# Optimization experiments

Hardware: AMD Instinct MI355X
Metric: run time of the kernel (lower is better)

## Reference

```python
import jax, jax.numpy as jnp
import numpy as np

N = 100000   # nodes
DIM = 128    # feature dim
E = 800000   # edges per hop
K = 4        # hops
BN_EPS = 1e-5


def setup_inputs() -> dict:
    key = jax.random.key(0)
    ks = jax.random.split(key, 24)
    inp = {}
    for i in range(K):
        inp[f"x{i}"] = jax.random.normal(ks[i], (N, DIM), dtype=jnp.float32)
    inp["edge_attr"] = jax.random.normal(ks[4], (E, DIM), dtype=jnp.float32)
    for i in range(K):
        inp[f"e{i}"] = jax.random.randint(ks[5 + i], (2, E), 0, N, dtype=jnp.int32)
    s1 = 1.0 / np.sqrt(DIM)
    s2 = 1.0 / np.sqrt(2 * DIM)
    inp["W1"] = jax.random.uniform(ks[9], (DIM, 2 * DIM), jnp.float32, -s1, s1)
    inp["b1"] = jax.random.uniform(ks[10], (2 * DIM,), jnp.float32, -s1, s1)
    inp["bn1_g"] = jnp.ones((2 * DIM,), jnp.float32)
    inp["bn1_b"] = jnp.zeros((2 * DIM,), jnp.float32)
    inp["W2"] = jax.random.uniform(ks[11], (2 * DIM, DIM), jnp.float32, -s2, s2)
    inp["b2"] = jax.random.uniform(ks[12], (DIM,), jnp.float32, -s2, s2)
    inp["bn2_g"] = jnp.ones((DIM,), jnp.float32)
    inp["bn2_b"] = jnp.zeros((DIM,), jnp.float32)
    inp["bn3_g"] = jnp.ones((DIM,), jnp.float32)
    inp["bn3_b"] = jnp.zeros((DIM,), jnp.float32)
    inp["eps_param"] = jnp.zeros((K + 1, DIM), jnp.float32)  # nn.Parameter(zeros)
    return inp


def _bn(h, g, b):
    # BatchNorm1d, train-mode math: batch mean / biased var per feature
    m = jnp.mean(h, axis=0)
    v = jnp.var(h, axis=0)
    return g * (h - m) * jax.lax.rsqrt(v + BN_EPS) + b


def _propagate(x, edge_index, edge_attr):
    # message: relu(x_j [+ edge_attr]); aggregate: scatter-add at dst
    msg = x[edge_index[0]]                      # [E, DIM] gather from src
    if edge_attr is not None:
        msg = msg + edge_attr
    msg = jax.nn.relu(msg)
    return jax.ops.segment_sum(msg, edge_index[1], num_segments=N)


def reference(x0, x1, x2, x3, edge_attr, e0, e1, e2, e3,
              W1, b1, bn1_g, bn1_b, W2, b2, bn2_g, bn2_b,
              bn3_g, bn3_b, eps_param):
    xs = [x0, x1, x2, x3]
    es = [e0, e1, e2, e3]
    result = (1.0 + eps_param[0]) * x0
    for i in range(K):
        ea = edge_attr if i == 0 else None
        result = result + (1.0 + eps_param[i + 1]) * _propagate(xs[i], es[i], ea)
    # GIN MLP: Linear -> BN -> ReLU -> Linear -> BN -> ReLU
    h = jax.nn.relu(_bn(result @ W1 + b1, bn1_g, bn1_b))
    h = jax.nn.relu(_bn(h @ W2 + b2, bn2_g, bn2_b))
    # outer ConvBlock: BN -> act (relu, not last layer); dropout in eval = identity
    h = jax.nn.relu(_bn(h, bn3_g, bn3_b))
    return h  # new x[0]; original also carries XX through unchanged
```

## Files before the change

### kernel.cpp

```cpp
#include <hip/hip_runtime.h>
#include <cstdint>
#include <cstddef>

#define NN 100000
#define D 128
#define NE 800000
#define BN_EPS 1e-5f

#define M4 (4 * NN)
#define CH 1000
#define NB 400
#define G64 1563

typedef __attribute__((ext_vector_type(4))) float f32x4;
typedef __attribute__((ext_vector_type(8))) short s16x8;

__device__ inline unsigned short f2bf(float f) {
  unsigned int u = __builtin_bit_cast(unsigned int, f);
  u += 0x7FFFu + ((u >> 16) & 1u);
  return (unsigned short)(u >> 16);
}

__global__ __launch_bounds__(256) void k_prep(const float* __restrict__ W1,
                                              const float* __restrict__ W2,
                                              unsigned short* __restrict__ W1T,
                                              unsigned short* __restrict__ W2T) {
  int i = blockIdx.x * 256 + threadIdx.x;
  if (i >= 32768) return;
  int k1 = i >> 8, n1 = i & 255;
  W1T[n1 * 128 + k1] = f2bf(W1[i]);
  int k2 = i >> 7, n2 = i & 127;
  W2T[n2 * 256 + k2] = f2bf(W2[i]);
}

__global__ __launch_bounds__(256) void k_count(
    const int* __restrict__ e0, const int* __restrict__ e1,
    const int* __restrict__ e2, const int* __restrict__ e3,
    unsigned int* __restrict__ pcount, unsigned char* __restrict__ wrank) {
  const int h = blockIdx.y;
  const int* e = h == 0 ? e0 : h == 1 ? e1 : h == 2 ? e2 : e3;
  const int eid = blockIdx.x * 256 + threadIdx.x;
  const int dst = e[NE + eid];
  unsigned int old = atomicAdd(&pcount[dst], 1u << (8 * h));
  wrank[h * NE + eid] = (unsigned char)((old >> (8 * h)) & 0xFFu);
}

__global__ __launch_bounds__(256) void k_scanA(const unsigned int* __restrict__ pcount,
                                               int* __restrict__ bsum) {
  __shared__ int red[256];
  const int b = blockIdx.x, t = threadIdx.x;
  int s = 0;
  if (t < 250) {
    unsigned int p = pcount[b * 250 + t];
    s = (int)((p & 0xFFu) + ((p >> 8) & 0xFFu) + ((p >> 16) & 0xFFu) + (p >> 24));
  }
  red[t] = s; __syncthreads();
  for (int off = 128; off > 0; off >>= 1) {
    if (t < off) red[t] += red[t + off];
    __syncthreads();
  }
  if (t == 0) bsum[b] = red[0];
}

__global__ __launch_bounds__(512) void k_scanB(const int* __restrict__ bsum,
                                               int* __restrict__ bpre) {
  __shared__ int s[512];
  const int t = threadIdx.x;
  const int v = (t < NB) ? bsum[t] : 0;
  s[t] = v; __syncthreads();
  for (int off = 1; off < 512; off <<= 1) {
    int x = s[t];
    if (t >= off) x += s[t - off];
    __syncthreads(); s[t] = x; __syncthreads();
  }
  if (t < NB) bpre[t] = s[t] - v;
}

__global__ __launch_bounds__(256) void k_scanC(const unsigned int* __restrict__ pcount,
                                               const int* __restrict__ bpre,
                                               int* __restrict__ offsets) {
  __shared__ int cnt[CH];
  __shared__ int part[256];
  const int b = blockIdx.x, t = threadIdx.x;
  if (t < 250) {
    unsigned int p = pcount[b * 250 + t];
    cnt[t * 4 + 0] = (int)(p & 0xFFu);
    cnt[t * 4 + 1] = (int)((p >> 8) & 0xFFu);
    cnt[t * 4 + 2] = (int)((p >> 16) & 0xFFu);
    cnt[t * 4 + 3] = (int)(p >> 24);
  }
  __syncthreads();
  int own = 0;
#pragma unroll
  for (int j = 0; j < 4; j++) {
    int idx = t * 4 + j;
    if (idx < CH) own += cnt[idx];
  }
  part[t] = own; __syncthreads();
  for (int off = 1; off < 256; off <<= 1) {
    int x = part[t];
    if (t >= off) x += part[t - off];
    __syncthreads(); part[t] = x; __syncthreads();
  }
  int run = bpre[b] + part[t] - own;
#pragma unroll
  for (int j = 0; j < 4; j++) {
    int idx = t * 4 + j;
    if (idx < CH) { offsets[b * CH + idx] = run; run += cnt[idx]; }
  }
  if (b == 0 && t == 0) offsets[M4] = 4 * NE;
}

__global__ __launch_bounds__(256) void k_place(
    const int* __restrict__ e0, const int* __restrict__ e1,
    const int* __restrict__ e2, const int* __restrict__ e3,
    const int* __restrict__ offsets, const unsigned char* __restrict__ wrank,
    int* __restrict__ srcs, int* __restrict__ eids) {
  const int h = blockIdx.y;
  const int* e = h == 0 ? e0 : h == 1 ? e1 : h == 2 ? e2 : e3;
  const int eid = blockIdx.x * 256 + threadIdx.x;
  const int src = e[eid];
  const int dst = e[NE + eid];
  const int pos = offsets[dst * 4 + h] + (int)wrank[h * NE + eid];
  srcs[pos] = src;
  if (h == 0) eids[pos] = eid;
}

__global__ __launch_bounds__(256) void k_gather(
    const float* __restrict__ x0, const float* __restrict__ x1,
    const float* __restrict__ x2, const float* __restrict__ x3,
    const float* __restrict__ edge_attr, const float* __restrict__ eps,
    const int* __restrict__ offsets, const int* __restrict__ srcs,
    const int* __restrict__ eids, unsigned short* __restrict__ result) {
  const int dst  = blockIdx.x * 4 + (threadIdx.x >> 6);
  const int lane = threadIdx.x & 63;
  const int d    = lane * 2;

  const int4 ob = *reinterpret_cast<const int4*>(offsets + 4 * dst);
  const int o0 = ob.x, b1 = ob.y, b2 = ob.z, b3 = ob.w;
  const int o4 = offsets[4 * dst + 4];

  float2 h0 = make_float2(0.f, 0.f);
  float2 h1 = make_float2(0.f, 0.f);
  float2 h2 = make_float2(0.f, 0.f);
  float2 h3 = make_float2(0.f, 0.f);

  {
    int j = o0;
    for (; j + 2 <= b1; j += 2) {
      const int p0 = srcs[j],     p1 = srcs[j + 1];
      const int q0 = eids[j],     q1 = eids[j + 1];
      float2 v0 = *reinterpret_cast<const float2*>(x0 + p0 * D + d);
      float2 w0 = *reinterpret_cast<const float2*>(edge_attr + (size_t)q0 * D + d);
      float2 v1 = *reinterpret_cast<const float2*>(x0 + p1 * D + d);
      float2 w1 = *reinterpret_cast<const float2*>(edge_attr + (size_t)q1 * D + d);
      h0.x += fmaxf(v0.x + w0.x, 0.f); h0.y += fmaxf(v0.y + w0.y, 0.f);
      h0.x += fmaxf(v1.x + w1.x, 0.f); h0.y += fmaxf(v1.y + w1.y, 0.f);
    }
    if (j < b1) {
      const int p = srcs[j];
      const int q = eids[j];
      float2 v = *reinterpret_cast<const float2*>(x0 + p * D + d);
      float2 w = *reinterpret_cast<const float2*>(edge_attr + (size_t)q * D + d);
      h0.x += fmaxf(v.x + w.x, 0.f); h0.y += fmaxf(v.y + w.y, 0.f);
    }
  }

#define HOP_LOOP(XP, ACC, BEG, END) do {                                       \
    int j_ = (BEG);                                                            \
    for (; j_ + 4 <= (END); j_ += 4) {                                         \
      const int p0_ = srcs[j_], p1_ = srcs[j_ + 1];                            \
      const int p2_ = srcs[j_ + 2], p3_ = srcs[j_ + 3];                        \
      float2 v0_ = *reinterpret_cast<const float2*>((XP) + p0_ * D + d);       \
      float2 v1_ = *reinterpret_cast<const float2*>((XP) + p1_ * D + d);       \
      float2 v2_ = *reinterpret_cast<const float2*>((XP) + p2_ * D + d);       \
      float2 v3_ = *reinterpret_cast<const float2*>((XP) + p3_ * D + d);       \
      ACC.x += fmaxf(v0_.x, 0.f); ACC.y += fmaxf(v0_.y, 0.f);                  \
      ACC.x += fmaxf(v1_.x, 0.f); ACC.y += fmaxf(v1_.y, 0.f);                  \
      ACC.x += fmaxf(v2_.x, 0.f); ACC.y += fmaxf(v2_.y, 0.f);                  \
      ACC.x += fmaxf(v3_.x, 0.f); ACC.y += fmaxf(v3_.y, 0.f);                  \
    }                                                                          \
    for (; j_ < (END); ++j_) {                                                 \
      const int p_ = srcs[j_];                                                 \
      float2 v_ = *reinterpret_cast<const float2*>((XP) + p_ * D + d);         \
      ACC.x += fmaxf(v_.x, 0.f); ACC.y += fmaxf(v_.y, 0.f);                    \
    }                                                                          \
  } while (0)

  HOP_LOOP(x1, h1, b1, b2);
  HOP_LOOP(x2, h2, b2, b3);
  HOP_LOOP(x3, h3, b3, o4);
#undef HOP_LOOP

  float2 e0v = *reinterpret_cast<const float2*>(eps + d);
  float2 s1 = *reinterpret_cast<const float2*>(eps + 1 * D + d);
  float2 s2 = *reinterpret_cast<const float2*>(eps + 2 * D + d);
  float2 s3 = *reinterpret_cast<const float2*>(eps + 3 * D + d);
  float2 s4 = *reinterpret_cast<const float2*>(eps + 4 * D + d);
  float2 xv = *reinterpret_cast<const float2*>(x0 + dst * D + d);

  float ax = (1.f + e0v.x) * xv.x + (1.f + s1.x) * h0.x + (1.f + s2.x) * h1.x
           + (1.f + s3.x) * h2.x + (1.f + s4.x) * h3.x;
  float ay = (1.f + e0v.y) * xv.y + (1.f + s1.y) * h0.y + (1.f + s2.y) * h1.y
           + (1.f + s3.y) * h2.y + (1.f + s4.y) * h3.y;

  reinterpret_cast<unsigned int*>(result)[dst * 64 + lane] =
      (unsigned int)f2bf(ax) | ((unsigned int)f2bf(ay) << 16);
}

__global__ __launch_bounds__(256) void k_gemm1(const unsigned short* __restrict__ Ab,
                                               const unsigned short* __restrict__ W1T,
                                               float* __restrict__ C) {
  const int lane = threadIdx.x & 63, wave = threadIdx.x >> 6;
  const int ln = lane & 15, lk = lane >> 4;
  const int m0 = blockIdx.x * 64 + wave * 16;
  const int arow = m0 + ln;
  const bool av = arow < NN;

  f32x4 acc[16];
#pragma unroll
  for (int t = 0; t < 16; t++) acc[t] = (f32x4)0.f;

#pragma unroll
  for (int kk = 0; kk < 4; kk++) {
    const int kb = kk * 32 + lk * 8;
    s16x8 a = (s16x8)(short)0;
    if (av) a = *reinterpret_cast<const s16x8*>(Ab + arow * 128 + kb);
#pragma unroll
    for (int t = 0; t < 16; t++) {
      s16x8 b = *reinterpret_cast<const s16x8*>(W1T + (t * 16 + ln) * 128 + kb);
      acc[t] = __builtin_amdgcn_mfma_f32_16x16x32_bf16(a, b, acc[t], 0, 0, 0);
    }
  }
#pragma unroll
  for (int t = 0; t < 16; t++) {
#pragma unroll
    for (int r = 0; r < 4; r++) {
      const int row = m0 + lk * 4 + r;
      if (row < NN) C[(size_t)row * 256 + t * 16 + ln] = acc[t][r];
    }
  }
}

__global__ __launch_bounds__(256) void k_gemm2(const float* __restrict__ t1,
                                               const unsigned short* __restrict__ W2T,
                                               const float* __restrict__ sc,
                                               const float* __restrict__ sh,
                                               float* __restrict__ C) {
  __shared__ float s1s[256], s1h[256];
  const int tid = threadIdx.x;
  if (tid < 256) { s1s[tid] = sc[tid]; s1h[tid] = sh[tid]; }
  __syncthreads();

  const int lane = tid & 63, wave = tid >> 6;
  const int ln = lane & 15, lk = lane >> 4;
  const int m0 = blockIdx.x * 64 + wave * 16;
  const int arow = m0 + ln;
  const bool av = arow < NN;

  f32x4 acc[8];
#pragma unroll
  for (int t = 0; t < 8; t++) acc[t] = (f32x4)0.f;

#pragma unroll
  for (int kk = 0; kk < 8; kk++) {
    const int kb = kk * 32 + lk * 8;
    float va[8];
    if (av) {
      *reinterpret_cast<float4*>(va)     = *reinterpret_cast<const float4*>(t1 + (size_t)arow * 256 + kb);
      *reinterpret_cast<float4*>(va + 4) = *reinterpret_cast<const float4*>(t1 + (size_t)arow * 256 + kb + 4);
    } else {
#pragma unroll
      for (int i = 0; i < 8; i++) va[i] = 0.f;
    }
    s16x8 a;
#pragma unroll
    for (int i = 0; i < 8; i++) {
      float v = fmaxf(fmaf(s1s[kb + i], va[i], s1h[kb + i]), 0.f);
      a[i] = (short)f2bf(v);
    }
#pragma unroll
    for (int t = 0; t < 8; t++) {
      s16x8 b = *reinterpret_cast<const s16x8*>(W2T + (t * 16 + ln) * 256 + kb);
      acc[t] = __builtin_amdgcn_mfma_f32_16x16x32_bf16(a, b, acc[t], 0, 0, 0);
    }
  }
#pragma unroll
  for (int t = 0; t < 8; t++) {
#pragma unroll
    for (int r = 0; r < 4; r++) {
      const int row = m0 + lk * 4 + r;
      if (row < NN) C[(size_t)row * 128 + t * 16 + ln] = acc[t][r];
    }
  }
}

template <int C, bool ACT>
__global__ __launch_bounds__(256) void k_colstats(const float* __restrict__ X,
                                                  const float* __restrict__ sc,
                                                  const float* __restrict__ sh,
                                                  float* __restrict__ sums,
                                                  float* __restrict__ sumsq) {
  const long total = (long)NN * C;
  const long stride = (long)gridDim.x * 256;
  const long start = (long)blockIdx.x * 256 + threadIdx.x;
  const int c = (int)(start & (C - 1));
  float scale = 0.f, shiftv = 0.f;
  if constexpr (ACT) { scale = sc[c]; shiftv = sh[c]; }
  float s = 0.f, q = 0.f;
  for (long idx = start; idx < total; idx += stride) {
    float v = X[idx];
    if constexpr (ACT) v = fmaxf(fmaf(scale, v, shiftv), 0.f);
    s += v;
    q = fmaf(v, v, q);
  }
  unsafeAtomicAdd(&sums[c], s);
  unsafeAtomicAdd(&sumsq[c], q);
}

template <int C>
__global__ void k_bnfinal(const float* __restrict__ sums, const float* __restrict__ sumsq,
                          const float* __restrict__ g, const float* __restrict__ b,
                          float* __restrict__ scale, float* __restrict__ shift) {
  int c = threadIdx.x;
  if (c >= C) return;
  float mean = sums[c] * (1.f / NN);
  float var  = sumsq[c] * (1.f / NN) - mean * mean;
  float rs   = rsqrtf(var + BN_EPS);
  float s    = g[c] * rs;
  scale[c] = s;
  shift[c] = b[c] - mean * s;
}

__global__ __launch_bounds__(256) void k_colstats3(const float* __restrict__ X,
                                                   const float* __restrict__ sums2,
                                                   const float* __restrict__ sumsq2,
                                                   const float* __restrict__ bn2_g,
                                                   const float* __restrict__ bn2_b,
                                                   float* __restrict__ sums3,
                                                   float* __restrict__ sumsq3) {
  const long total = (long)NN * 128;
  const long stride = (long)gridDim.x * 256;
  const long start = (long)blockIdx.x * 256 + threadIdx.x;
  const int c = (int)(start & 127);
  float mean = sums2[c] * (1.f / NN);
  float var  = sumsq2[c] * (1.f / NN) - mean * mean;
  float rs   = rsqrtf(var + BN_EPS);
  float scale = bn2_g[c] * rs;
  float shiftv = bn2_b[c] - mean * scale;
  float s = 0.f, q = 0.f;
  for (long idx = start; idx < total; idx += stride) {
    float v = fmaxf(fmaf(scale, X[idx], shiftv), 0.f);
    s += v;
    q = fmaf(v, v, q);
  }
  unsafeAtomicAdd(&sums3[c], s);
  unsafeAtomicAdd(&sumsq3[c], q);
}

__global__ __launch_bounds__(256) void k_final(float* __restrict__ t2,
                                               const float* __restrict__ sums2,
                                               const float* __restrict__ sumsq2,
                                               const float* __restrict__ bn2_g,
                                               const float* __restrict__ bn2_b,
                                               const float* __restrict__ sums3,
                                               const float* __restrict__ sumsq3,
                                               const float* __restrict__ bn3_g,
                                               const float* __restrict__ bn3_b) {
  int i4 = blockIdx.x * 256 + threadIdx.x;
  if (i4 >= NN * D / 4) return;
  int d = (i4 & 31) * 4;
  float4 v = reinterpret_cast<float4*>(t2)[i4];
  float o[4];
  float* vv = reinterpret_cast<float*>(&v);
#pragma unroll
  for (int j = 0; j < 4; j++) {
    int c = d + j;
    float m2 = sums2[c] * (1.f / NN);
    float va2 = sumsq2[c] * (1.f / NN) - m2 * m2;
    float r2 = rsqrtf(va2 + BN_EPS);
    float a2 = bn2_g[c] * r2;
    float h2 = bn2_b[c] - m2 * a2;
    float m3 = sums3[c] * (1.f / NN);
    float va3 = sumsq3[c] * (1.f / NN) - m3 * m3;
    float r3 = rsqrtf(va3 + BN_EPS);
    float a3 = bn3_g[c] * r3;
    float h3 = bn3_b[c] - m3 * a3;
    o[j] = fmaxf(fmaf(a3, fmaxf(fmaf(a2, vv[j], h2), 0.f), h3), 0.f);
  }
  reinterpret_cast<float4*>(t2)[i4] = make_float4(o[0], o[1], o[2], o[3]);
}

extern "C" void kernel_launch(void* const* d_in, const int* in_sizes, int n_in,
                              void* d_out, int out_size, void* d_ws, size_t ws_size,
                              hipStream_t stream) {
  const float* x0 = (const float*)d_in[0];
  const float* x1 = (const float*)d_in[1];
  const float* x2 = (const float*)d_in[2];
  const float* x3 = (const float*)d_in[3];
  const float* edge_attr = (const float*)d_in[4];
  const int* e0 = (const int*)d_in[5];
  const int* e1 = (const int*)d_in[6];
  const int* e2 = (const int*)d_in[7];
  const int* e3 = (const int*)d_in[8];
  const float* W1 = (const float*)d_in[9];
  const float* bn1_g = (const float*)d_in[11];
  const float* bn1_b = (const float*)d_in[12];
  const float* W2 = (const float*)d_in[13];
  const float* bn2_g = (const float*)d_in[15];
  const float* bn2_b = (const float*)d_in[16];
  const float* bn3_g = (const float*)d_in[17];
  const float* bn3_b = (const float*)d_in[18];
  const float* eps = (const float*)d_in[19];

  char* ws = (char*)d_ws;
  unsigned short* resultb = (unsigned short*)ws;
  float* t1 = (float*)(ws + (size_t)NN * D * 2);
  float* stats = t1 + (size_t)NN * 256;
  float* sums1  = stats;
  float* sumsq1 = sums1 + 256;
  float* sums2  = sumsq1 + 256;
  float* sumsq2 = sums2 + 128;
  float* sums3  = sumsq2 + 128;
  float* sumsq3 = sums3 + 128;
  float* scale1 = sumsq3 + 128;
  float* shift1 = scale1 + 256;
  unsigned short* W1T = (unsigned short*)(shift1 + 256);
  unsigned short* W2T = W1T + 32768;
  unsigned int* pcount = (unsigned int*)(W2T + 32768);
  unsigned char* wrank = (unsigned char*)(pcount + NN);

  int* offsets = (int*)t1;
  int* bsum    = offsets + M4 + 1;
  int* bpre    = bsum + NB;
  int* srcs    = bpre + NB;
  int* eids    = srcs + 4 * NE;

  float* t2 = (float*)d_out;

  hipMemsetAsync(pcount, 0, NN * sizeof(unsigned int), stream);
  hipMemsetAsync(stats, 0, 1024 * sizeof(float), stream);

  k_prep<<<128, 256, 0, stream>>>(W1, W2, W1T, W2T);

  k_count<<<dim3(NE / 256, 4), 256, 0, stream>>>(e0, e1, e2, e3, pcount, wrank);
  k_scanA<<<NB, 256, 0, stream>>>(pcount, bsum);
  k_scanB<<<1, 512, 0, stream>>>(bsum, bpre);
  k_scanC<<<NB, 256, 0, stream>>>(pcount, bpre, offsets);
  k_place<<<dim3(NE / 256, 4), 256, 0, stream>>>(e0, e1, e2, e3, offsets, wrank, srcs, eids);

  k_gather<<<NN / 4, 256, 0, stream>>>(x0, x1, x2, x3, edge_attr, eps,
                                       offsets, srcs, eids, resultb);

  k_gemm1<<<G64, 256, 0, stream>>>(resultb, W1T, t1);
  k_colstats<256, false><<<512, 256, 0, stream>>>(t1, nullptr, nullptr, sums1, sumsq1);
  k_bnfinal<256><<<1, 256, 0, stream>>>(sums1, sumsq1, bn1_g, bn1_b, scale1, shift1);
  k_gemm2<<<G64, 256, 0, stream>>>(t1, W2T, scale1, shift1, t2);
  k_colstats<128, false><<<512, 256, 0, stream>>>(t2, nullptr, nullptr, sums2, sumsq2);
  k_colstats3<<<512, 256, 0, stream>>>(t2, sums2, sumsq2, bn2_g, bn2_b, sums3, sumsq3);
  k_final<<<NN * D / 4 / 256, 256, 0, stream>>>(t2, sums2, sumsq2, bn2_g, bn2_b,
                                                sums3, sumsq3, bn3_g, bn3_b);
}
```

Before: 877.1 us.

## Fuse BN column statistics into GEMM epilogues and store hidden activations as bf16

Column sum and sum-of-squares for BN1 and BN2 are now accumulated in the GEMM epilogues through LDS atomics followed by global atomics, which removes the separate colstats and bnfinal kernels. GEMM2 computes the BN1 scale and shift inline. The 256-wide intermediate t1 is stored as bf16 instead of fp32, halving its write and read traffic at some precision cost. The first hop's gather now reads the source index through eids into e0 instead of a separate srcs array, uses nontemporal loads for edge_attr, and unrolls by 4. GEMM blocks grow to 512 threads.

```diff
diff --git a/kernel.cpp b/kernel.cpp
--- a/kernel.cpp
+++ b/kernel.cpp
@@ -10,15 +10,23 @@
 #define M4 (4 * NN)
 #define CH 1000
 #define NB 400
-#define G64 1563
+#define GB 782
 
 typedef __attribute__((ext_vector_type(4))) float f32x4;
+typedef __attribute__((ext_vector_type(2))) float f32x2;
 typedef __attribute__((ext_vector_type(8))) short s16x8;
 
 __device__ inline unsigned short f2bf(float f) {
   unsigned int u = __builtin_bit_cast(unsigned int, f);
   u += 0x7FFFu + ((u >> 16) & 1u);
   return (unsigned short)(u >> 16);
+}
+__device__ inline float bf2f(unsigned short u) {
+  unsigned int x = ((unsigned int)u) << 16;
+  return __builtin_bit_cast(float, x);
+}
+__device__ inline f32x2 ntload2(const float* p) {
+  return __builtin_nontemporal_load(reinterpret_cast<const f32x2*>(p));
 }
 
 __global__ __launch_bounds__(256) void k_prep(const float* __restrict__ W1,
@@ -119,19 +127,22 @@
   const int h = blockIdx.y;
   const int* e = h == 0 ? e0 : h == 1 ? e1 : h == 2 ? e2 : e3;
   const int eid = blockIdx.x * 256 + threadIdx.x;
-  const int src = e[eid];
   const int dst = e[NE + eid];
   const int pos = offsets[dst * 4 + h] + (int)wrank[h * NE + eid];
-  srcs[pos] = src;
-  if (h == 0) eids[pos] = eid;
+  if (h == 0) {
+    eids[pos] = eid;
+  } else {
+    srcs[pos] = e[eid];
+  }
 }
 
 __global__ __launch_bounds__(256) void k_gather(
     const float* __restrict__ x0, const float* __restrict__ x1,
     const float* __restrict__ x2, const float* __restrict__ x3,
     const float* __restrict__ edge_attr, const float* __restrict__ eps,
-    const int* __restrict__ offsets, const int* __restrict__ srcs,
-    const int* __restrict__ eids, unsigned short* __restrict__ result) {
+    const int* __restrict__ e0, const int* __restrict__ offsets,
+    const int* __restrict__ srcs, const int* __restrict__ eids,
+    unsigned short* __restrict__ result) {
   const int dst  = blockIdx.x * 4 + (threadIdx.x >> 6);
   const int lane = threadIdx.x & 63;
   const int d    = lane * 2;
@@ -147,22 +158,28 @@
 
   {
     int j = o0;
-    for (; j + 2 <= b1; j += 2) {
-      const int p0 = srcs[j],     p1 = srcs[j + 1];
-      const int q0 = eids[j],     q1 = eids[j + 1];
+    for (; j + 4 <= b1; j += 4) {
+      const int q0 = eids[j], q1 = eids[j + 1], q2 = eids[j + 2], q3 = eids[j + 3];
+      const int p0 = e0[q0], p1 = e0[q1], p2 = e0[q2], p3 = e0[q3];
+      f32x2 w0 = ntload2(edge_attr + (size_t)q0 * D + d);
+      f32x2 w1 = ntload2(edge_attr + (size_t)q1 * D + d);
+      f32x2 w2 = ntload2(edge_attr + (size_t)q2 * D + d);
+      f32x2 w3 = ntload2(edge_attr + (size_t)q3 * D + d);
       float2 v0 = *reinterpret_cast<const float2*>(x0 + p0 * D + d);
-      float2 w0 = *reinterpret_cast<const float2*>(edge_attr + (size_t)q0 * D + d);
       float2 v1 = *reinterpret_cast<const float2*>(x0 + p1 * D + d);
-      float2 w1 = *reinterpret_cast<const float2*>(edge_attr + (size_t)q1 * D + d);
-      h0.x += fmaxf(v0.x + w0.x, 0.f); h0.y += fmaxf(v0.y + w0.y, 0.f);
-      h0.x += fmaxf(v1.x + w1.x, 0.f); h0.y += fmaxf(v1.y + w1.y, 0.f);
-    }
-    if (j < b1) {
-      const int p = srcs[j];
+      float2 v2 = *reinterpret_cast<const float2*>(x0 + p2 * D + d);
+      float2 v3 = *reinterpret_cast<const float2*>(x0 + p3 * D + d);
+      h0.x += fmaxf(v0.x + w0[0], 0.f); h0.y += fmaxf(v0.y + w0[1], 0.f);
+      h0.x += fmaxf(v1.x + w1[0], 0.f); h0.y += fmaxf(v1.y + w1[1], 0.f);
+      h0.x += fmaxf(v2.x + w2[0], 0.f); h0.y += fmaxf(v2.y + w2[1], 0.f);
+      h0.x += fmaxf(v3.x + w3[0], 0.f); h0.y += fmaxf(v3.y + w3[1], 0.f);
+    }
+    for (; j < b1; ++j) {
       const int q = eids[j];
+      const int p = e0[q];
+      f32x2 w = ntload2(edge_attr + (size_t)q * D + d);
       float2 v = *reinterpret_cast<const float2*>(x0 + p * D + d);
-      float2 w = *reinterpret_cast<const float2*>(edge_attr + (size_t)q * D + d);
-      h0.x += fmaxf(v.x + w.x, 0.f); h0.y += fmaxf(v.y + w.y, 0.f);
+      h0.x += fmaxf(v.x + w[0], 0.f); h0.y += fmaxf(v.y + w[1], 0.f);
     }
   }
 
@@ -208,12 +225,19 @@
       (unsigned int)f2bf(ax) | ((unsigned int)f2bf(ay) << 16);
 }
 
-__global__ __launch_bounds__(256) void k_gemm1(const unsigned short* __restrict__ Ab,
+__global__ __launch_bounds__(512) void k_gemm1(const unsigned short* __restrict__ Ab,
                                                const unsigned short* __restrict__ W1T,
-                                               float* __restrict__ C) {
-  const int lane = threadIdx.x & 63, wave = threadIdx.x >> 6;
+                                               unsigned short* __restrict__ t1b,
+                                               float* __restrict__ sums1,
+                                               float* __restrict__ sumsq1) {
+  __shared__ float ls[256], lq[256];
+  const int tid = threadIdx.x;
+  if (tid < 256) { ls[tid] = 0.f; lq[tid] = 0.f; }
+  __syncthreads();
+
+  const int lane = tid & 63, wave = tid >> 6;
   const int ln = lane & 15, lk = lane >> 4;
-  const int m0 = blockIdx.x * 64 + wave * 16;
+  const int m0 = blockIdx.x * 128 + wave * 16;
   const int arow = m0 + ln;
   const bool av = arow < NN;
 
@@ -234,27 +258,51 @@
   }
 #pragma unroll
   for (int t = 0; t < 16; t++) {
+    float cs = 0.f, cq = 0.f;
 #pragma unroll
     for (int r = 0; r < 4; r++) {
       const int row = m0 + lk * 4 + r;
-      if (row < NN) C[(size_t)row * 256 + t * 16 + ln] = acc[t][r];
-    }
-  }
-}
-
-__global__ __launch_bounds__(256) void k_gemm2(const float* __restrict__ t1,
+      float v = acc[t][r];
+      if (row < NN) t1b[(size_t)row * 256 + t * 16 + ln] = f2bf(v);
+      cs += v;
+      cq = fmaf(v, v, cq);
+    }
+    atomicAdd(&ls[t * 16 + ln], cs);
+    atomicAdd(&lq[t * 16 + ln], cq);
+  }
+  __syncthreads();
+  if (tid < 256) {
+    unsafeAtomicAdd(&sums1[tid], ls[tid]);
+    unsafeAtomicAdd(&sumsq1[tid], lq[tid]);
+  }
+}
+
+__global__ __launch_bounds__(512) void k_gemm2(const unsigned short* __restrict__ t1b,
                                                const unsigned short* __restrict__ W2T,
-                                               const float* __restrict__ sc,
-                                               const float* __restrict__ sh,
-                                               float* __restrict__ C) {
+                                               const float* __restrict__ sums1,
+                                               const float* __restrict__ sumsq1,
+                                               const float* __restrict__ bn1_g,
+                                               const float* __restrict__ bn1_b,
+                                               float* __restrict__ C,
+                                               float* __restrict__ sums2,
+                                               float* __restrict__ sumsq2) {
   __shared__ float s1s[256], s1h[256];
+  __shared__ float ls[128], lq[128];
   const int tid = threadIdx.x;
-  if (tid < 256) { s1s[tid] = sc[tid]; s1h[tid] = sh[tid]; }
+  if (tid < 256) {
+    float mean = sums1[tid] * (1.f / NN);
+    float var  = sumsq1[tid] * (1.f / NN) - mean * mean;
+    float rs   = rsqrtf(var + BN_EPS);
+    float s    = bn1_g[tid] * rs;
+    s1s[tid] = s;
+    s1h[tid] = bn1_b[tid] - mean * s;
+  }
+  if (tid < 128) { ls[tid] = 0.f; lq[tid] = 0.f; }
   __syncthreads();
 
   const int lane = tid & 63, wave = tid >> 6;
   const int ln = lane & 15, lk = lane >> 4;
-  const int m0 = blockIdx.x * 64 + wave * 16;
+  const int m0 = blockIdx.x * 128 + wave * 16;
   const int arow = m0 + ln;
   const bool av = arow < NN;
 
@@ -265,19 +313,14 @@
 #pragma unroll
   for (int kk = 0; kk < 8; kk++) {
     const int kb = kk * 32 + lk * 8;
-    float va[8];
-    if (av) {
-      *reinterpret_cast<float4*>(va)     = *reinterpret_cast<const float4*>(t1 + (size_t)arow * 256 + kb);
-      *reinterpret_cast<float4*>(va + 4) = *reinterpret_cast<const float4*>(t1 + (size_t)arow * 256 + kb + 4);
-    } else {
-#pragma unroll
-      for (int i = 0; i < 8; i++) va[i] = 0.f;
-    }
+    s16x8 raw = (s16x8)(short)0;
+    if (av) raw = *reinterpret_cast<const s16x8*>(t1b + (size_t)arow * 256 + kb);
     s16x8 a;
 #pragma unroll
     for (int i = 0; i < 8; i++) {
-      float v = fmaxf(fmaf(s1s[kb + i], va[i], s1h[kb + i]), 0.f);
-      a[i] = (short)f2bf(v);
+      const int col = kb + i;
+      float v = fmaxf(fmaf(s1s[col], bf2f((unsigned short)raw[i]), s1h[col]), 0.f);
+      a[i] = (short)f2bf(av ? v : 0.f);
     }
 #pragma unroll
     for (int t = 0; t < 8; t++) {
@@ -287,49 +330,25 @@
   }
 #pragma unroll
   for (int t = 0; t < 8; t++) {
+    float cs = 0.f, cq = 0.f;
 #pragma unroll
     for (int r = 0; r < 4; r++) {
       const int row = m0 + lk * 4 + r;
-      if (row < NN) C[(size_t)row * 128 + t * 16 + ln] = acc[t][r];
-    }
-  }
-}
-
-template <int C, bool ACT>
-__global__ __launch_bounds__(256) void k_colstats(const float* __restrict__ X,
-                                                  const float* __restrict__ sc,
-                                                  const float* __restrict__ sh,
-                                                  float* __restrict__ sums,
-                                                  float* __restrict__ sumsq) {
-  const long total = (long)NN * C;
-  const long stride = (long)gridDim.x * 256;
-  const long start = (long)blockIdx.x * 256 + threadIdx.x;
-  const int c = (int)(start & (C - 1));
-  float scale = 0.f, shiftv = 0.f;
-  if constexpr (ACT) { scale = sc[c]; shiftv = sh[c]; }
-  float s = 0.f, q = 0.f;
-  for (long idx = start; idx < total; idx += stride) {
-    float v = X[idx];
-    if constexpr (ACT) v = fmaxf(fmaf(scale, v, shiftv), 0.f);
-    s += v;
-    q = fmaf(v, v, q);
-  }
-  unsafeAtomicAdd(&sums[c], s);
-  unsafeAtomicAdd(&sumsq[c], q);
-}
-
-template <int C>
-__global__ void k_bnfinal(const float* __restrict__ sums, const float* __restrict__ sumsq,
-                          const float* __restrict__ g, const float* __restrict__ b,
-                          float* __restrict__ scale, float* __restrict__ shift) {
-  int c = threadIdx.x;
-  if (c >= C) return;
-  float mean = sums[c] * (1.f / NN);
-  float var  = sumsq[c] * (1.f / NN) - mean * mean;
-  float rs   = rsqrtf(var + BN_EPS);
-  float s    = g[c] * rs;
-  scale[c] = s;
-  shift[c] = b[c] - mean * s;
+      float v = acc[t][r];
+      if (row < NN) {
+        C[(size_t)row * 128 + t * 16 + ln] = v;
+        cs += v;
+        cq = fmaf(v, v, cq);
+      }
+    }
+    atomicAdd(&ls[t * 16 + ln], cs);
+    atomicAdd(&lq[t * 16 + ln], cq);
+  }
+  __syncthreads();
+  if (tid < 128) {
+    unsafeAtomicAdd(&sums2[tid], ls[tid]);
+    unsafeAtomicAdd(&sumsq2[tid], lq[tid]);
+  }
 }
 
 __global__ __launch_bounds__(256) void k_colstats3(const float* __restrict__ X,
@@ -415,22 +434,20 @@
 
   char* ws = (char*)d_ws;
   unsigned short* resultb = (unsigned short*)ws;
-  float* t1 = (float*)(ws + (size_t)NN * D * 2);
-  float* stats = t1 + (size_t)NN * 256;
+  unsigned short* t1b = (unsigned short*)(ws + (size_t)NN * D * 2);
+  float* stats = (float*)(ws + (size_t)NN * D * 2 + (size_t)NN * 256 * 2);
   float* sums1  = stats;
   float* sumsq1 = sums1 + 256;
   float* sums2  = sumsq1 + 256;
   float* sumsq2 = sums2 + 128;
   float* sums3  = sumsq2 + 128;
   float* sumsq3 = sums3 + 128;
-  float* scale1 = sumsq3 + 128;
-  float* shift1 = scale1 + 256;
-  unsigned short* W1T = (unsigned short*)(shift1 + 256);
+  unsigned short* W1T = (unsigned short*)(sumsq3 + 128);
   unsigned short* W2T = W1T + 32768;
   unsigned int* pcount = (unsigned int*)(W2T + 32768);
   unsigned char* wrank = (unsigned char*)(pcount + NN);
 
-  int* offsets = (int*)t1;
+  int* offsets = (int*)t1b;
   int* bsum    = offsets + M4 + 1;
   int* bpre    = bsum + NB;
   int* srcs    = bpre + NB;
@@ -449,14 +466,12 @@
   k_scanC<<<NB, 256, 0, stream>>>(pcount, bpre, offsets);
   k_place<<<dim3(NE / 256, 4), 256, 0, stream>>>(e0, e1, e2, e3, offsets, wrank, srcs, eids);
 
-  k_gather<<<NN / 4, 256, 0, stream>>>(x0, x1, x2, x3, edge_attr, eps,
+  k_gather<<<NN / 4, 256, 0, stream>>>(x0, x1, x2, x3, edge_attr, eps, e0,
                                        offsets, srcs, eids, resultb);
 
-  k_gemm1<<<G64, 256, 0, stream>>>(resultb, W1T, t1);
-  k_colstats<256, false><<<512, 256, 0, stream>>>(t1, nullptr, nullptr, sums1, sumsq1);
-  k_bnfinal<256><<<1, 256, 0, stream>>>(sums1, sumsq1, bn1_g, bn1_b, scale1, shift1);
-  k_gemm2<<<G64, 256, 0, stream>>>(t1, W2T, scale1, shift1, t2);
-  k_colstats<128, false><<<512, 256, 0, stream>>>(t2, nullptr, nullptr, sums2, sumsq2);
+  k_gemm1<<<GB, 512, 0, stream>>>(resultb, W1T, t1b, sums1, sumsq1);
+  k_gemm2<<<GB, 512, 0, stream>>>(t1b, W2T, sums1, sumsq1, bn1_g, bn1_b,
+                                  t2, sums2, sumsq2);
   k_colstats3<<<512, 256, 0, stream>>>(t2, sums2, sumsq2, bn2_g, bn2_b, sums3, sumsq3);
   k_final<<<NN * D / 4 / 256, 256, 0, stream>>>(t2, sums2, sumsq2, bn2_g, bn2_b,
                                                 sums3, sumsq3, bn3_g, bn3_b);
```

Result: no change. 861.7 us (-1.8%).
